# Performance work log

Hardware: AMD Instinct MI355X
Metric: run time of the kernel (lower is better)

Reference implementation:

```python
import jax, jax.numpy as jnp
import numpy as np

B, S, D = 4, 2048, 1024
H, DK = 16, 64
NEG = -1e9


def setup_inputs() -> dict:
    key = jax.random.key(0)
    ks = jax.random.split(key, 6)
    hidden_states = jax.random.normal(ks[0], (B, S, D), dtype=jnp.float32)
    # evidence-constrained mask: causal mask plus random evidence restriction
    causal = jnp.tril(jnp.ones((S, S), dtype=bool))
    evid = jax.random.bernoulli(ks[1], 0.7, (S, S))
    allowed = causal & (evid | jnp.eye(S, dtype=bool))  # diag always allowed
    attention_mask = jnp.where(allowed, 0.0, NEG).astype(jnp.float32)
    scale = 0.02
    Wq = jax.random.normal(ks[2], (H * DK, D), dtype=jnp.float32) * scale
    Wk = jax.random.normal(ks[3], (H * DK, D), dtype=jnp.float32) * scale
    Wv = jax.random.normal(ks[4], (H * DK, D), dtype=jnp.float32) * scale
    Wo = jax.random.normal(ks[5], (D, H * DK), dtype=jnp.float32) * scale
    return {"hidden_states": hidden_states, "attention_mask": attention_mask,
            "Wq": Wq, "Wk": Wk, "Wv": Wv, "Wo": Wo}


def reference(hidden_states, attention_mask, Wq, Wk, Wv, Wo):
    b, s, _ = hidden_states.shape
    # nn.Linear(bias=False): y = x @ W.T ; reshape to (B,H,S,DK)
    def proj(x, W):
        y = jnp.einsum('bsd,ed->bse', x, W)
        return y.reshape(b, s, H, DK).transpose(0, 2, 1, 3)
    q = proj(hidden_states, Wq)
    k = proj(hidden_states, Wk)
    v = proj(hidden_states, Wv)
    logits = jnp.einsum('bhqd,bhkd->bhqk', q, k) / jnp.sqrt(jnp.float32(DK))
    logits = logits + attention_mask[None, None, :, :]
    attn = jax.nn.softmax(logits, axis=-1)
    ctx = jnp.einsum('bhqk,bhkd->bhqd', attn, v)
    ctx = ctx.transpose(0, 2, 1, 3).reshape(b, s, H * DK)
    out = jnp.einsum('bse,de->bsd', ctx, Wo)
    return out
```

## Files before the change

kernel.cpp:

```cpp
#include <hip/hip_runtime.h>
#include <hip/hip_bf16.h>
#include <math.h>

#define B_  4
#define S_  2048
#define D_  1024
#define H_  16
#define DK_ 64
#define M_  (B_*S_)
#define E_  (H_*DK_)
#define LOG2E  1.4426950408889634f
#define QSCALE 0.18033688011112042f

typedef short  bf16x8 __attribute__((ext_vector_type(8)));
typedef float  f32x4  __attribute__((ext_vector_type(4)));
typedef unsigned short u16;
typedef unsigned int   u32;
typedef unsigned long long u64;

extern "C" __device__ float __ocml_native_exp2_f32(float);

__device__ __forceinline__ u16 f2b(float x) {
    __hip_bfloat16 h = __float2bfloat16(x);
    return *(u16*)&h;
}

__device__ __forceinline__ u32 cvtpk(float lo, float hi) {
    u32 r;
    asm("v_cvt_pk_bf16_f32 %0, %1, %2" : "=v"(r) : "v"(lo), "v"(hi));
    return r;
}

__device__ __forceinline__ void async16(const u16* g, u16* l) {
    __builtin_amdgcn_global_load_lds(
        (const __attribute__((address_space(1))) unsigned int*)g,
        (__attribute__((address_space(3))) unsigned int*)l, 16, 0, 0);
}

#define XN8 (M_ * D_ / 8)
#define WN8 (E_ * D_ / 8)
__global__ __launch_bounds__(256)
void cvt_all(const float* __restrict__ X,
             const float* __restrict__ Wq, const float* __restrict__ Wk,
             const float* __restrict__ Wv, const float* __restrict__ Wo,
             u16* __restrict__ Xb,
             u16* __restrict__ Wqb, u16* __restrict__ Wkb,
             u16* __restrict__ Wvb, u16* __restrict__ Wob) {
    int idx = blockIdx.x * 256 + threadIdx.x;
    const float* s; u16* d; int off;
    if (idx < XN8) { s = X; d = Xb; off = idx; }
    else {
        int j = idx - XN8;
        int which = j / WN8; off = j - which * WN8;
        s = which == 0 ? Wq : which == 1 ? Wk : which == 2 ? Wv : Wo;
        d = which == 0 ? Wqb : which == 1 ? Wkb : which == 2 ? Wvb : Wob;
    }
    const float4* s4 = (const float4*)s;
    float4 a = s4[2 * off], b = s4[2 * off + 1];
    u16 o[8] = {f2b(a.x), f2b(a.y), f2b(a.z), f2b(a.w),
                f2b(b.x), f2b(b.y), f2b(b.z), f2b(b.w)};
    *(uint4*)(d + (size_t)8 * off) = *(const uint4*)o;
}

__global__ __launch_bounds__(256)
void maskcvt(const float* __restrict__ mask, u32* __restrict__ bits) {
    const int w   = threadIdx.x >> 6;
    const int lane = threadIdx.x & 63;
    const int row = blockIdx.x * 4 + w;
    const float* mr = mask + (size_t)row * S_;
    u64* br = (u64*)(bits + (size_t)row * (S_ / 32));
    #pragma unroll
    for (int i = 0; i < S_ / 64; i++) {
        float v = mr[i * 64 + lane];
        u64 bal = __ballot(v == 0.0f);
        if (lane == 0) br[i] = bal;
    }
}

__device__ __forceinline__ void gemm_core(
    const u16* __restrict__ Ag, const u16* __restrict__ Bg, int K,
    int bm, int bn, u16* As, u16* Bs, f32x4 (&acc)[4][4])
{
    const int tid  = threadIdx.x;
    const int w    = tid >> 6, lane = tid & 63;
    const int l15  = lane & 15, quad = lane >> 4;
    const int wm   = (w >> 1) * 64, wn = (w & 1) * 64;
    const int srow = lane >> 3;
    const int sg   = (lane & 7) ^ srow;
    const int sx   = l15 & 7;

    for (int k0 = 0; k0 < K; k0 += 64) {
        __syncthreads();
        #pragma unroll
        for (int i = 0; i < 4; i++) {
            const int row = w * 32 + i * 8 + srow;
            async16(Ag + (size_t)(bm + row) * K + k0 + sg * 8,
                    As + (size_t)(w * 32 + i * 8) * 64);
            async16(Bg + (size_t)(bn + row) * K + k0 + sg * 8,
                    Bs + (size_t)(w * 32 + i * 8) * 64);
        }
        __syncthreads();

        #pragma unroll
        for (int s = 0; s < 2; s++) {
            bf16x8 af[4], bf[4];
            #pragma unroll
            for (int i = 0; i < 4; i++)
                af[i] = *(const bf16x8*)(As + (size_t)(wm + i * 16 + l15) * 64
                                            + (((s * 4 + quad) ^ sx) * 8));
            #pragma unroll
            for (int j = 0; j < 4; j++)
                bf[j] = *(const bf16x8*)(Bs + (size_t)(wn + j * 16 + l15) * 64
                                            + (((s * 4 + quad) ^ sx) * 8));
            #pragma unroll
            for (int i = 0; i < 4; i++)
                #pragma unroll
                for (int j = 0; j < 4; j++)
                    acc[i][j] = __builtin_amdgcn_mfma_f32_16x16x32_bf16(af[i], bf[j], acc[i][j], 0, 0, 0);
        }
    }
}

__global__ __launch_bounds__(256)
void gemm_qkv(const u16* __restrict__ Xb,
              const u16* __restrict__ Wqb, const u16* __restrict__ Wkb,
              const u16* __restrict__ Wvb,
              u16* __restrict__ Qm, u16* __restrict__ Km, u16* __restrict__ Vt)
{
    __shared__ u16 As[128 * 64];
    __shared__ u16 Bs[128 * 64];
    const int bm    = blockIdx.x * 128;
    const int nb    = blockIdx.y;
    const int which = nb >> 3;
    const int col0  = (nb & 7) * 128;
    const u16* Bg = which == 0 ? Wqb : which == 1 ? Wkb : Wvb;

    f32x4 acc[4][4] = {};
    gemm_core(Xb, Bg, D_, bm, col0, As, Bs, acc);

    const int tid = threadIdx.x;
    const int w   = tid >> 6, lane = tid & 63;
    const int l15 = lane & 15, quad = lane >> 4;
    const int wm  = (w >> 1) * 64, wn = (w & 1) * 64;

    if (which == 2) {
        #pragma unroll
        for (int i = 0; i < 4; i++)
            #pragma unroll
            for (int j = 0; j < 4; j++) {
                int c    = col0 + wn + j * 16 + l15;
                int tok0 = bm + wm + i * 16 + quad * 4;
                int u    = tok0 & 63;
                int perm = (u & 32) | ((u & 12) << 1) | ((u & 16) >> 2);
                int tp   = (tok0 & (2047 & ~63)) | perm;
                u16 pk[4] = {f2b(acc[i][j][0]), f2b(acc[i][j][1]),
                             f2b(acc[i][j][2]), f2b(acc[i][j][3])};
                size_t idx = (((size_t)((tok0 >> 11) * E_ + c)) << 11) + tp;
                *(uint2*)(Vt + idx) = *(const uint2*)pk;
            }
    } else {
        u16* Cm = which == 0 ? Qm : Km;
        const float sc = which == 0 ? QSCALE : 1.0f;
        #pragma unroll
        for (int i = 0; i < 4; i++)
            #pragma unroll
            for (int j = 0; j < 4; j++)
                #pragma unroll
                for (int r = 0; r < 4; r++) {
                    int row = bm + wm + i * 16 + quad * 4 + r;
                    int c   = col0 + wn + j * 16 + l15;
                    Cm[(size_t)row * E_ + c] = f2b(acc[i][j][r] * sc);
                }
    }
}

__global__ __launch_bounds__(256)
void gemm_out(const u16* __restrict__ Cmx, const u16* __restrict__ Wob,
              float* __restrict__ out)
{
    __shared__ u16 As[128 * 64];
    __shared__ u16 Bs[128 * 64];
    const int bm = blockIdx.x * 128;
    const int bn = blockIdx.y * 128;

    f32x4 acc[4][4] = {};
    gemm_core(Cmx, Wob, E_, bm, bn, As, Bs, acc);

    const int tid = threadIdx.x;
    const int w   = tid >> 6, lane = tid & 63;
    const int l15 = lane & 15, quad = lane >> 4;
    const int wm  = (w >> 1) * 64, wn = (w & 1) * 64;
    #pragma unroll
    for (int i = 0; i < 4; i++)
        #pragma unroll
        for (int j = 0; j < 4; j++)
            #pragma unroll
            for (int r = 0; r < 4; r++)
                out[(size_t)(bm + wm + i * 16 + quad * 4 + r) * D_ + bn + wn + j * 16 + l15]
                    = acc[i][j][r];
}

__global__ __launch_bounds__(512)
void flash_attn(const u16* __restrict__ Q, const u16* __restrict__ Kc,
                const u16* __restrict__ Vt, const u32* __restrict__ bits,
                u16* __restrict__ ctx)
{
    const int bh  = blockIdx.x;
    const int qt  = (gridDim.y - 1) - blockIdx.y;
    const int b   = bh >> 4, h = bh & 15;
    const int tid = threadIdx.x;
    const int w   = tid >> 6, lane = tid & 63;
    const int l15 = lane & 15, quad = lane >> 4;
    const int q0  = qt * 128;
    const int nkt = 2 * qt + 2;

    __shared__ u16 Ks[2][64 * 64];
    __shared__ u16 Vs[2][64 * 64];

    const u16* qb = Q + ((size_t)(b * S_ + q0 + w * 16 + l15)) * E_ + h * DK_;
    bf16x8 qf0 = *(const bf16x8*)(qb + quad * 8);
    bf16x8 qf1 = *(const bf16x8*)(qb + 32 + quad * 8);

    f32x4 acc[4] = {};
    f32x4 accL = {};

    const int sr = lane >> 3;
    const int sg = (lane & 7) ^ sr;
    const int sx = l15 & 7;

    const u32* mrow = bits + (size_t)(q0 + w * 16 + l15) * (S_ / 32);
    const u16* kg = Kc + ((size_t)(b * S_ + w * 8 + sr)) * E_ + h * DK_ + sg * 8;
    const u16* vg = Vt + ((size_t)(bh * DK_ + w * 8 + sr)) * S_ + sg * 8;

    async16(kg, &Ks[0][w * 512]); kg += (size_t)64 * E_;
    async16(vg, &Vs[0][w * 512]); vg += 64;
    u64 mw_next = *(const u64*)mrow;

    union { u32 w4[4]; bf16x8 v; } ones;
    ones.w4[0] = ones.w4[1] = ones.w4[2] = ones.w4[3] = 0x3F803F80u;

    int cur = 0;
    for (int kt = 0; kt < nkt; ++kt) {
        const int nxt = cur ^ 1;
        __syncthreads();
        u64 mw = mw_next;
        if (kt + 1 < nkt) {
            async16(kg, &Ks[nxt][w * 512]); kg += (size_t)64 * E_;
            async16(vg, &Vs[nxt][w * 512]); vg += 64;
            mw_next = *(const u64*)(mrow + ((kt + 1) << 1));
        }

        const u16* Kb = Ks[cur];
        f32x4 st[4] = {};
        #pragma unroll
        for (int t = 0; t < 4; t++) {
            bf16x8 kf0 = *(const bf16x8*)(Kb + (t * 16 + l15) * 64 + ((quad ^ sx) * 8));
            bf16x8 kf1 = *(const bf16x8*)(Kb + (t * 16 + l15) * 64 + (((4 + quad) ^ sx) * 8));
            st[t] = __builtin_amdgcn_mfma_f32_16x16x32_bf16(kf0, qf0, st[t], 0, 0, 0);
            st[t] = __builtin_amdgcn_mfma_f32_16x16x32_bf16(kf1, qf1, st[t], 0, 0, 0);
        }

        const u64 m2 = mw >> (quad * 4);
        const u32 mlo = (u32)m2, mhi = (u32)(m2 >> 32);
        const u32 nib[4] = { mlo & 0xF, (mlo >> 16) & 0xF,
                             mhi & 0xF, (mhi >> 16) & 0xF };
        #pragma unroll
        for (int t = 0; t < 4; t++) {
            st[t][0] = (nib[t] & 1) ? __ocml_native_exp2_f32(st[t][0]) : 0.0f;
            st[t][1] = (nib[t] & 2) ? __ocml_native_exp2_f32(st[t][1]) : 0.0f;
            st[t][2] = (nib[t] & 4) ? __ocml_native_exp2_f32(st[t][2]) : 0.0f;
            st[t][3] = (nib[t] & 8) ? __ocml_native_exp2_f32(st[t][3]) : 0.0f;
        }

        const u16* Vb = Vs[cur];
        #pragma unroll
        for (int sb = 0; sb < 2; sb++) {
            union { u32 w4[4]; bf16x8 v; } pu;
            pu.w4[0] = cvtpk(st[2 * sb][0],     st[2 * sb][1]);
            pu.w4[1] = cvtpk(st[2 * sb][2],     st[2 * sb][3]);
            pu.w4[2] = cvtpk(st[2 * sb + 1][0], st[2 * sb + 1][1]);
            pu.w4[3] = cvtpk(st[2 * sb + 1][2], st[2 * sb + 1][3]);
            accL = __builtin_amdgcn_mfma_f32_16x16x32_bf16(pu.v, ones.v, accL, 0, 0, 0);
            #pragma unroll
            for (int nt = 0; nt < 4; nt++) {
                bf16x8 vf = *(const bf16x8*)(Vb + (nt * 16 + l15) * 64
                                                + (((4 * sb + quad) ^ sx) * 8));
                acc[nt] = __builtin_amdgcn_mfma_f32_16x16x32_bf16(pu.v, vf, acc[nt], 0, 0, 0);
            }
        }
        cur = nxt;
    }

    #pragma unroll
    for (int r = 0; r < 4; r++) {
        float ir = 1.0f / accL[r];
        size_t orow = ((size_t)(b * S_ + q0 + w * 16 + quad * 4 + r)) * E_ + h * DK_;
        #pragma unroll
        for (int nt = 0; nt < 4; nt++)
            ctx[orow + nt * 16 + l15] = f2b(acc[nt][r] * ir);
    }
}

extern "C" void kernel_launch(void* const* d_in, const int* in_sizes, int n_in,
                              void* d_out, int out_size, void* d_ws, size_t ws_size,
                              hipStream_t stream) {
    const float* X    = (const float*)d_in[0];
    const float* mask = (const float*)d_in[1];
    const float* Wq   = (const float*)d_in[2];
    const float* Wk   = (const float*)d_in[3];
    const float* Wv   = (const float*)d_in[4];
    const float* Wo   = (const float*)d_in[5];
    float* out = (float*)d_out;

    char* p = (char*)d_ws;
    u16* Qm  = (u16*)p; p += (size_t)M_ * E_ * 2;
    u16* Km  = (u16*)p; p += (size_t)M_ * E_ * 2;
    u16* Vt  = (u16*)p; p += (size_t)M_ * E_ * 2;
    u16* Wqb = (u16*)p; p += (size_t)E_ * D_ * 2;
    u16* Wkb = (u16*)p; p += (size_t)E_ * D_ * 2;
    u16* Wvb = (u16*)p; p += (size_t)E_ * D_ * 2;
    u16* Wob = (u16*)p; p += (size_t)D_ * E_ * 2;
    u32* Mb  = (u32*)p; p += (size_t)S_ * (S_ / 32) * 4;
    u16* Xb  = (u16*)p;
    u16* Cm  = Xb;

    cvt_all<<<(XN8 + 4 * WN8 + 255) / 256, 256, 0, stream>>>(
        X, Wq, Wk, Wv, Wo, Xb, Wqb, Wkb, Wvb, Wob);
    maskcvt<<<S_ / 4, 256, 0, stream>>>(mask, Mb);

    gemm_qkv<<<dim3(M_ / 128, 24), 256, 0, stream>>>(Xb, Wqb, Wkb, Wvb, Qm, Km, Vt);

    flash_attn<<<dim3(B_ * H_, S_ / 128), 512, 0, stream>>>(Qm, Km, Vt, Mb, Cm);

    gemm_out<<<dim3(M_ / 128, D_ / 128), 256, 0, stream>>>(Cm, Wob, out);
}
```

Before: 262.8 us.

## Use 256x256 double-buffered QKV GEMM and fold mask conversion into cvt kernel

Replaces the 128x128 single-buffered QKV projection GEMM with a 256x256-tile, 8-wave kernel. It double-buffers LDS through async global-to-LDS loads, interleaves prefetch with MFMA quadrants, raises wave priority around the MFMAs, and swizzles the block index for L2 locality. The mask-to-bitmask conversion moves into the weight/activation conversion kernel to save one launch. The larger tile improves operand reuse but uses 128KB of LDS and yields only 384 blocks, which may lower occupancy and wave balance across CUs.

```diff
diff --git a/kernel.cpp b/kernel.cpp
--- a/kernel.cpp
+++ b/kernel.cpp
@@ -39,13 +39,30 @@
 
 #define XN8 (M_ * D_ / 8)
 #define WN8 (E_ * D_ / 8)
+#define CVTB ((XN8 + 4 * WN8) / 256)
 __global__ __launch_bounds__(256)
 void cvt_all(const float* __restrict__ X,
              const float* __restrict__ Wq, const float* __restrict__ Wk,
              const float* __restrict__ Wv, const float* __restrict__ Wo,
+             const float* __restrict__ mask,
              u16* __restrict__ Xb,
              u16* __restrict__ Wqb, u16* __restrict__ Wkb,
-             u16* __restrict__ Wvb, u16* __restrict__ Wob) {
+             u16* __restrict__ Wvb, u16* __restrict__ Wob,
+             u32* __restrict__ bits) {
+    if (blockIdx.x >= CVTB) {
+        const int w    = threadIdx.x >> 6;
+        const int lane = threadIdx.x & 63;
+        const int row  = (blockIdx.x - CVTB) * 4 + w;
+        const float* mr = mask + (size_t)row * S_;
+        u64* br = (u64*)(bits + (size_t)row * (S_ / 32));
+        #pragma unroll
+        for (int i = 0; i < S_ / 64; i++) {
+            float v = mr[i * 64 + lane];
+            u64 bal = __ballot(v == 0.0f);
+            if (lane == 0) br[i] = bal;
+        }
+        return;
+    }
     int idx = blockIdx.x * 256 + threadIdx.x;
     const float* s; u16* d; int off;
     if (idx < XN8) { s = X; d = Xb; off = idx; }
@@ -60,21 +77,6 @@
     u16 o[8] = {f2b(a.x), f2b(a.y), f2b(a.z), f2b(a.w),
                 f2b(b.x), f2b(b.y), f2b(b.z), f2b(b.w)};
     *(uint4*)(d + (size_t)8 * off) = *(const uint4*)o;
-}
-
-__global__ __launch_bounds__(256)
-void maskcvt(const float* __restrict__ mask, u32* __restrict__ bits) {
-    const int w   = threadIdx.x >> 6;
-    const int lane = threadIdx.x & 63;
-    const int row = blockIdx.x * 4 + w;
-    const float* mr = mask + (size_t)row * S_;
-    u64* br = (u64*)(bits + (size_t)row * (S_ / 32));
-    #pragma unroll
-    for (int i = 0; i < S_ / 64; i++) {
-        float v = mr[i * 64 + lane];
-        u64 bal = __ballot(v == 0.0f);
-        if (lane == 0) br[i] = bal;
-    }
 }
 
 __device__ __forceinline__ void gemm_core(
@@ -121,56 +123,186 @@
     }
 }
 
-__global__ __launch_bounds__(256)
-void gemm_qkv(const u16* __restrict__ Xb,
-              const u16* __restrict__ Wqb, const u16* __restrict__ Wkb,
-              const u16* __restrict__ Wvb,
-              u16* __restrict__ Qm, u16* __restrict__ Km, u16* __restrict__ Vt)
+__global__ __launch_bounds__(512, 2)
+void gemm_qkv256(const u16* __restrict__ Xb,
+                 const u16* __restrict__ Wqb, const u16* __restrict__ Wkb,
+                 const u16* __restrict__ Wvb,
+                 u16* __restrict__ Qm, u16* __restrict__ Km, u16* __restrict__ Vt)
 {
-    __shared__ u16 As[128 * 64];
-    __shared__ u16 Bs[128 * 64];
-    const int bm    = blockIdx.x * 128;
-    const int nb    = blockIdx.y;
-    const int which = nb >> 3;
-    const int col0  = (nb & 7) * 128;
-    const u16* Bg = which == 0 ? Wqb : which == 1 ? Wkb : Wvb;
-
-    f32x4 acc[4][4] = {};
-    gemm_core(Xb, Bg, D_, bm, col0, As, Bs, acc);
-
-    const int tid = threadIdx.x;
-    const int w   = tid >> 6, lane = tid & 63;
-    const int l15 = lane & 15, quad = lane >> 4;
-    const int wm  = (w >> 1) * 64, wn = (w & 1) * 64;
+    __shared__ u16 As[2][256 * 64];
+    __shared__ u16 Bs[2][256 * 64];
+
+    int bid = blockIdx.y * gridDim.x + blockIdx.x;
+    bid = (bid & 7) * 48 + (bid >> 3);
+    const int bm    = (bid & 31) * 256;
+    const int by    = bid >> 5;
+    const int which = by >> 2;
+    const int col0  = (by & 3) * 256;
+    const u16* __restrict__ Bg = which == 0 ? Wqb : which == 1 ? Wkb : Wvb;
+
+    const int tid  = threadIdx.x;
+    const int w    = tid >> 6, lane = tid & 63;
+    const int l15  = lane & 15, quad = lane >> 4;
+    const int wr   = w >> 2, wc = w & 3;
+    const int sr   = lane >> 3;
+    const int sg   = (lane & 7) ^ sr;
+    const int sx   = l15 & 7;
+
+    f32x4 acc[8][4] = {};
+
+    const u16* agA = Xb + (size_t)(bm   + w * 8 + sr) * D_ + sg * 8;
+    const u16* bgB = Bg + (size_t)(col0 + w * 8 + sr) * D_ + sg * 8;
+
+#define STG_A(b, h, kt) do { \
+        const u16* s_ = agA + (size_t)((h) * 128) * D_ + (kt) * 64; \
+        u16* d_ = &As[b][((h) * 128 + w * 8) * 64]; \
+        async16(s_, d_); \
+        async16(s_ + (size_t)64 * D_, d_ + 64 * 64); } while (0)
+#define STG_B(b, h, kt) do { \
+        const u16* s_ = bgB + (size_t)((h) * 128) * D_ + (kt) * 64; \
+        u16* d_ = &Bs[b][((h) * 128 + w * 8) * 64]; \
+        async16(s_, d_); \
+        async16(s_ + (size_t)64 * D_, d_ + 64 * 64); } while (0)
+#define WAITV4() do { \
+        asm volatile("s_waitcnt vmcnt(4)" ::: "memory"); \
+        __builtin_amdgcn_sched_barrier(0); \
+        __builtin_amdgcn_s_barrier(); \
+        __builtin_amdgcn_sched_barrier(0); } while (0)
+
+    STG_A(0, 0, 0); STG_B(0, 0, 0); STG_A(0, 1, 0); STG_B(0, 1, 0);
+
+    for (int T = 0; T < D_ / 64; ++T) {
+        const int cb = T & 1, nb = cb ^ 1;
+        const u16* AsB = As[cb];
+        const u16* BsB = Bs[cb];
+        const bool pre = (T + 1 < D_ / 64);
+        const int kt1 = T + 1;
+
+        bf16x8 a[4][2], bq[2][2];
+
+        WAITV4();
+        if (pre) STG_A(nb, 0, kt1);
+        #pragma unroll
+        for (int fm = 0; fm < 4; fm++)
+            #pragma unroll
+            for (int kh = 0; kh < 2; kh++)
+                a[fm][kh] = *(const bf16x8*)(AsB + (wr * 64 + fm * 16 + l15) * 64
+                                                 + (((kh * 4 + quad) ^ sx) * 8));
+        #pragma unroll
+        for (int fn = 0; fn < 2; fn++)
+            #pragma unroll
+            for (int kh = 0; kh < 2; kh++)
+                bq[fn][kh] = *(const bf16x8*)(BsB + (wc * 32 + fn * 16 + l15) * 64
+                                                  + (((kh * 4 + quad) ^ sx) * 8));
+        __builtin_amdgcn_s_setprio(1);
+        #pragma unroll
+        for (int fm = 0; fm < 4; fm++)
+            #pragma unroll
+            for (int fn = 0; fn < 2; fn++)
+                #pragma unroll
+                for (int kh = 0; kh < 2; kh++)
+                    acc[fm][fn] = __builtin_amdgcn_mfma_f32_16x16x32_bf16(
+                        a[fm][kh], bq[fn][kh], acc[fm][fn], 0, 0, 0);
+        __builtin_amdgcn_s_setprio(0);
+
+        WAITV4();
+        if (pre) STG_B(nb, 0, kt1);
+        #pragma unroll
+        for (int fm = 0; fm < 4; fm++)
+            #pragma unroll
+            for (int kh = 0; kh < 2; kh++)
+                a[fm][kh] = *(const bf16x8*)(AsB + (128 + wr * 64 + fm * 16 + l15) * 64
+                                                 + (((kh * 4 + quad) ^ sx) * 8));
+        __builtin_amdgcn_s_setprio(1);
+        #pragma unroll
+        for (int fm = 0; fm < 4; fm++)
+            #pragma unroll
+            for (int fn = 0; fn < 2; fn++)
+                #pragma unroll
+                for (int kh = 0; kh < 2; kh++)
+                    acc[4 + fm][fn] = __builtin_amdgcn_mfma_f32_16x16x32_bf16(
+                        a[fm][kh], bq[fn][kh], acc[4 + fm][fn], 0, 0, 0);
+        __builtin_amdgcn_s_setprio(0);
+
+        WAITV4();
+        if (pre) STG_A(nb, 1, kt1);
+        #pragma unroll
+        for (int fn = 0; fn < 2; fn++)
+            #pragma unroll
+            for (int kh = 0; kh < 2; kh++)
+                bq[fn][kh] = *(const bf16x8*)(BsB + (128 + wc * 32 + fn * 16 + l15) * 64
+                                                  + (((kh * 4 + quad) ^ sx) * 8));
+        __builtin_amdgcn_s_setprio(1);
+        #pragma unroll
+        for (int fm = 0; fm < 4; fm++)
+            #pragma unroll
+            for (int fn = 0; fn < 2; fn++)
+                #pragma unroll
+                for (int kh = 0; kh < 2; kh++)
+                    acc[4 + fm][2 + fn] = __builtin_amdgcn_mfma_f32_16x16x32_bf16(
+                        a[fm][kh], bq[fn][kh], acc[4 + fm][2 + fn], 0, 0, 0);
+        __builtin_amdgcn_s_setprio(0);
+
+        if (pre) STG_B(nb, 1, kt1);
+        #pragma unroll
+        for (int fm = 0; fm < 4; fm++)
+            #pragma unroll
+            for (int kh = 0; kh < 2; kh++)
+                a[fm][kh] = *(const bf16x8*)(AsB + (wr * 64 + fm * 16 + l15) * 64
+                                                 + (((kh * 4 + quad) ^ sx) * 8));
+        __builtin_amdgcn_s_setprio(1);
+        #pragma unroll
+        for (int fm = 0; fm < 4; fm++)
+            #pragma unroll
+            for (int fn = 0; fn < 2; fn++)
+                #pragma unroll
+                for (int kh = 0; kh < 2; kh++)
+                    acc[fm][2 + fn] = __builtin_amdgcn_mfma_f32_16x16x32_bf16(
+                        a[fm][kh], bq[fn][kh], acc[fm][2 + fn], 0, 0, 0);
+        __builtin_amdgcn_s_setprio(0);
+    }
+#undef STG_A
+#undef STG_B
+#undef WAITV4
 
     if (which == 2) {
         #pragma unroll
-        for (int i = 0; i < 4; i++)
-            #pragma unroll
-            for (int j = 0; j < 4; j++) {
-                int c    = col0 + wn + j * 16 + l15;
-                int tok0 = bm + wm + i * 16 + quad * 4;
-                int u    = tok0 & 63;
-                int perm = (u & 32) | ((u & 12) << 1) | ((u & 16) >> 2);
-                int tp   = (tok0 & (2047 & ~63)) | perm;
-                u16 pk[4] = {f2b(acc[i][j][0]), f2b(acc[i][j][1]),
-                             f2b(acc[i][j][2]), f2b(acc[i][j][3])};
-                size_t idx = (((size_t)((tok0 >> 11) * E_ + c)) << 11) + tp;
-                *(uint2*)(Vt + idx) = *(const uint2*)pk;
-            }
+        for (int mh = 0; mh < 2; mh++)
+            #pragma unroll
+            for (int fm = 0; fm < 4; fm++)
+                #pragma unroll
+                for (int nh = 0; nh < 2; nh++)
+                    #pragma unroll
+                    for (int fn = 0; fn < 2; fn++) {
+                        int tok0 = bm + mh * 128 + wr * 64 + fm * 16 + quad * 4;
+                        int c    = col0 + nh * 128 + wc * 32 + fn * 16 + l15;
+                        f32x4 v  = acc[mh * 4 + fm][nh * 2 + fn];
+                        int u    = tok0 & 63;
+                        int perm = (u & 32) | ((u & 12) << 1) | ((u & 16) >> 2);
+                        int tp   = (tok0 & (2047 & ~63)) | perm;
+                        u16 pk[4] = {f2b(v[0]), f2b(v[1]), f2b(v[2]), f2b(v[3])};
+                        size_t idx = (((size_t)((tok0 >> 11) * E_ + c)) << 11) + tp;
+                        *(uint2*)(Vt + idx) = *(const uint2*)pk;
+                    }
     } else {
         u16* Cm = which == 0 ? Qm : Km;
         const float sc = which == 0 ? QSCALE : 1.0f;
         #pragma unroll
-        for (int i = 0; i < 4; i++)
-            #pragma unroll
-            for (int j = 0; j < 4; j++)
-                #pragma unroll
-                for (int r = 0; r < 4; r++) {
-                    int row = bm + wm + i * 16 + quad * 4 + r;
-                    int c   = col0 + wn + j * 16 + l15;
-                    Cm[(size_t)row * E_ + c] = f2b(acc[i][j][r] * sc);
-                }
+        for (int mh = 0; mh < 2; mh++)
+            #pragma unroll
+            for (int fm = 0; fm < 4; fm++)
+                #pragma unroll
+                for (int nh = 0; nh < 2; nh++)
+                    #pragma unroll
+                    for (int fn = 0; fn < 2; fn++) {
+                        f32x4 v = acc[mh * 4 + fm][nh * 2 + fn];
+                        int c   = col0 + nh * 128 + wc * 32 + fn * 16 + l15;
+                        #pragma unroll
+                        for (int r = 0; r < 4; r++) {
+                            int row = bm + mh * 128 + wr * 64 + fm * 16 + quad * 4 + r;
+                            Cm[(size_t)row * E_ + c] = f2b(v[r] * sc);
+                        }
+                    }
     }
 }
 
@@ -324,11 +456,10 @@
     u16* Xb  = (u16*)p;
     u16* Cm  = Xb;
 
-    cvt_all<<<(XN8 + 4 * WN8 + 255) / 256, 256, 0, stream>>>(
-        X, Wq, Wk, Wv, Wo, Xb, Wqb, Wkb, Wvb, Wob);
-    maskcvt<<<S_ / 4, 256, 0, stream>>>(mask, Mb);
-
-    gemm_qkv<<<dim3(M_ / 128, 24), 256, 0, stream>>>(Xb, Wqb, Wkb, Wvb, Qm, Km, Vt);
+    cvt_all<<<CVTB + 512, 256, 0, stream>>>(
+        X, Wq, Wk, Wv, Wo, mask, Xb, Wqb, Wkb, Wvb, Wob, Mb);
+
+    gemm_qkv256<<<dim3(32, 12), 512, 0, stream>>>(Xb, Wqb, Wkb, Wvb, Qm, Km, Vt);
 
     flash_attn<<<dim3(B_ * H_, S_ / 128), 512, 0, stream>>>(Qm, Km, Vt, Mb, Cm);
 
```

New measurement: 289.6 us. +10.2%, slower.
